# Kernel optimization log

Hardware: AMD Instinct MI355X
Metric: run time of the kernel (lower is better)

## Reference

```python
import jax, jax.numpy as jnp
import numpy as np

EMBED_DIM = 1024
NUM_HEADS = 16
HEAD_DIM = EMBED_DIM // NUM_HEADS


def setup_inputs() -> dict:
    key = jax.random.key(0)
    ks = jax.random.split(key, 9)
    B, N, D = 2, 2048, EMBED_DIM
    s = 1.0 / np.sqrt(D)
    return {
        "x": jax.random.normal(ks[0], (B, N, D), jnp.float32),
        "Wq": jax.random.normal(ks[1], (D, D), jnp.float32) * s,
        "bq": jax.random.normal(ks[2], (D,), jnp.float32) * 0.01,
        "Wk": jax.random.normal(ks[3], (D, D), jnp.float32) * s,
        "bk": jax.random.normal(ks[4], (D,), jnp.float32) * 0.01,
        "Wv": jax.random.normal(ks[5], (D, D), jnp.float32) * s,
        "bv": jax.random.normal(ks[6], (D,), jnp.float32) * 0.01,
        "Wo": jax.random.normal(ks[7], (D, D), jnp.float32) * s,
        "bo": jax.random.normal(ks[8], (D,), jnp.float32) * 0.01,
    }


def reference(x, Wq, bq, Wk, bk, Wv, bv, Wo, bo):
    B, N, D = x.shape
    H, Hd = NUM_HEADS, HEAD_DIM
    # QKV projections (Linear: x @ W^T + b), split heads -> [B, H, N, Hd]
    q = (x @ Wq.T + bq).reshape(B, N, H, Hd).transpose(0, 2, 1, 3)
    k = (x @ Wk.T + bk).reshape(B, N, H, Hd).transpose(0, 2, 1, 3)
    v = (x @ Wv.T + bv).reshape(B, N, H, Hd).transpose(0, 2, 1, 3)
    scale = 1.0 / np.sqrt(Hd)
    scores = jnp.einsum("bhqd,bhkd->bhqk", q, k) * scale  # [B,H,N,N]
    attn = jax.nn.softmax(scores.astype(jnp.float32), axis=-1).astype(scores.dtype)
    out = jnp.einsum("bhqk,bhkd->bhqd", attn, v)  # [B,H,N,Hd]
    out = out.transpose(0, 2, 1, 3).reshape(B, N, D)
    return out @ Wo.T + bo
```

## Files before the change

kernel.cpp:

```cpp
#include <hip/hip_runtime.h>
#include <hip/hip_bf16.h>

typedef __attribute__((ext_vector_type(8))) short short8;
typedef __attribute__((ext_vector_type(4))) float f32x4;
typedef __attribute__((ext_vector_type(4))) unsigned short us4;

static __device__ __forceinline__ unsigned short f2bf(float f) {
    union { float f; unsigned u; } v; v.f = f;
    unsigned r = (v.u + 0x7FFFu + ((v.u >> 16) & 1u)) >> 16;
    return (unsigned short)r;
}
static __device__ __forceinline__ unsigned pk2(float a, float b) {
    union { float f; unsigned u; } x, y; x.f = a; y.f = b;
    unsigned lo = (x.u + 0x7FFFu + ((x.u >> 16) & 1u)) >> 16;
    unsigned hi = (y.u + 0x7FFFu + ((y.u >> 16) & 1u)) >> 16;
    return lo | (hi << 16);
}
static __device__ __forceinline__ unsigned pk2f(float a, float b) {
    union { float f; unsigned u; } x, y; x.f = a; y.f = b;
    return ((x.u + 0x8000u) >> 16) | ((y.u + 0x8000u) & 0xFFFF0000u);
}

#if __has_builtin(__builtin_amdgcn_exp2f)
#define EXP2(x) __builtin_amdgcn_exp2f(x)
#else
#define EXP2(x) exp2f(x)
#endif

static __device__ __forceinline__ void gld16(const unsigned short* g, unsigned short* l) {
    __builtin_amdgcn_global_load_lds(
        (const __attribute__((address_space(1))) void*)g,
        (__attribute__((address_space(3))) void*)l, 16, 0, 0);
}

#define QSCALE (0.125f * 1.44269504f)

__global__ __launch_bounds__(256) void convert_all(
    const float* __restrict__ x,  const float* __restrict__ wq,
    const float* __restrict__ wk, const float* __restrict__ wv,
    const float* __restrict__ wo, const float* __restrict__ bq,
    const float* __restrict__ bk, const float* __restrict__ bv,
    unsigned short* __restrict__ xbf, unsigned short* __restrict__ wqkv,
    unsigned short* __restrict__ wobf, float* __restrict__ bqkv)
{
    const int NX4 = (4096 * 1024) / 4;
    const int NW4 = (1024 * 1024) / 4;
    int i = blockIdx.x * 256 + threadIdx.x;
    if (i < NX4) {
        float4 v = ((const float4*)x)[i];
        us4 o = { f2bf(v.x), f2bf(v.y), f2bf(v.z), f2bf(v.w) };
        ((us4*)xbf)[i] = o;
    } else if (i < NX4 + 3 * NW4) {
        int j = i - NX4;
        const float* src = (j < NW4) ? wq + 4 * j
                         : (j < 2 * NW4) ? wk + 4 * (j - NW4)
                         : wv + 4 * (j - 2 * NW4);
        float4 v = *(const float4*)src;
        us4 o = { f2bf(v.x), f2bf(v.y), f2bf(v.z), f2bf(v.w) };
        ((us4*)wqkv)[j] = o;
    } else if (i < NX4 + 4 * NW4) {
        int j = i - NX4 - 3 * NW4;
        float4 v = ((const float4*)wo)[j];
        us4 o = { f2bf(v.x), f2bf(v.y), f2bf(v.z), f2bf(v.w) };
        ((us4*)wobf)[j] = o;
    } else if (i < NX4 + 4 * NW4 + 768) {
        int j = i - NX4 - 4 * NW4;
        const float* src = (j < 256) ? bq + 4 * j
                         : (j < 512) ? bk + 4 * (j - 256)
                         : bv + 4 * (j - 512);
        ((float4*)bqkv)[j] = *(const float4*)src;
    }
}

template <int MODE>
__global__ __launch_bounds__(256) void gemm_bt(
    const unsigned short* __restrict__ A, const unsigned short* __restrict__ B,
    const float* __restrict__ bias,
    unsigned short* __restrict__ Qb, unsigned short* __restrict__ Kb,
    unsigned short* __restrict__ Vtb, float* __restrict__ Cout, int Mtiles)
{
    __shared__ __attribute__((aligned(16))) unsigned short As[8192];
    __shared__ __attribute__((aligned(16))) unsigned short Bs[8192];
    const int tid = threadIdx.x, lane = tid & 63, wave = tid >> 6;
    const int bm = blockIdx.x % Mtiles, bn = blockIdx.x / Mtiles;
    const int m0 = bm * 128, n0 = bn * 128;
    const int wr = wave >> 1, wc = wave & 1;
    const int lo = lane & 15, g = lane >> 4;

    f32x4 acc[4][4];
#pragma unroll
    for (int i = 0; i < 4; ++i)
#pragma unroll
        for (int j = 0; j < 4; ++j) acc[i][j] = (f32x4){0.f, 0.f, 0.f, 0.f};

    for (int kt = 0; kt < 16; ++kt) {
        const int k0 = kt * 64;
#pragma unroll
        for (int p = 0; p < 4; ++p) {
            int off = (p * 256 + tid) * 8;
            int k8l = off >> 10, m = (off >> 3) & 127;
            const unsigned short* srcA;
            if (MODE == 0) {
                srcA = A + (size_t)(m0 + m) * 1024 + k0 + k8l * 8;
            } else {
                int gr = m0 + m, b = gr >> 11, n = gr & 2047;
                srcA = A + ((size_t)((b << 4) + kt) * 2048 + n) * 64 + k8l * 8;
            }
            gld16(srcA, &As[off]);
            gld16(B + (size_t)(n0 + m) * 1024 + k0 + k8l * 8, &Bs[off]);
        }
        __syncthreads();
        short8 af[4][2], bf[4][2];
#pragma unroll
        for (int i = 0; i < 4; ++i)
#pragma unroll
            for (int kc = 0; kc < 2; ++kc) {
                af[i][kc] = *(const short8*)&As[((kc * 4 + g) * 128 + wr * 64 + i * 16 + lo) * 8];
                bf[i][kc] = *(const short8*)&Bs[((kc * 4 + g) * 128 + wc * 64 + i * 16 + lo) * 8];
            }
#pragma unroll
        for (int kc = 0; kc < 2; ++kc)
#pragma unroll
            for (int i = 0; i < 4; ++i)
#pragma unroll
                for (int j = 0; j < 4; ++j)
                    acc[i][j] = __builtin_amdgcn_mfma_f32_16x16x32_bf16(
                        af[i][kc], bf[j][kc], acc[i][j], 0, 0, 0);
        __syncthreads();
    }

    if (MODE == 0) {
        const int sect = n0 >> 10;
#pragma unroll
        for (int i = 0; i < 4; ++i)
#pragma unroll
            for (int j = 0; j < 4; ++j) {
                int gc = n0 + wc * 64 + j * 16 + lo;
                int d = gc & 1023, h = d >> 6, hd = d & 63;
                float bv = bias[gc];
                int nb = m0 + wr * 64 + i * 16 + g * 4;
                int b = nb >> 11, n = nb & 2047;
                size_t hb = (size_t)((b << 4) + h) * 131072;
                if (sect == 0) {
#pragma unroll
                    for (int r = 0; r < 4; ++r)
                        Qb[hb + (size_t)(n + r) * 64 + hd] =
                            f2bf((acc[i][j][r] + bv) * QSCALE);
                } else if (sect == 1) {
#pragma unroll
                    for (int r = 0; r < 4; ++r)
                        Kb[hb + (size_t)(hd >> 3) * 16384 + (size_t)(n + r) * 8 + (hd & 7)] =
                            f2bf(acc[i][j][r] + bv);
                } else {
                    uint2 w;
                    w.x = pk2(acc[i][j][0] + bv, acc[i][j][1] + bv);
                    w.y = pk2(acc[i][j][2] + bv, acc[i][j][3] + bv);
                    *(uint2*)&Vtb[hb + (size_t)(n >> 3) * 512 + (size_t)hd * 8 + (n & 7)] = w;
                }
            }
    } else {
#pragma unroll
        for (int i = 0; i < 4; ++i)
#pragma unroll
            for (int j = 0; j < 4; ++j)
#pragma unroll
                for (int r = 0; r < 4; ++r) {
                    int gr = m0 + wr * 64 + i * 16 + g * 4 + r;
                    int gc = n0 + wc * 64 + j * 16 + lo;
                    Cout[(size_t)gr * 1024 + gc] = acc[i][j][r] + bias[gc];
                }
    }
}

__global__ __launch_bounds__(256, 2) void attn_kernel(
    const unsigned short* __restrict__ Qb, const unsigned short* __restrict__ Kb,
    const unsigned short* __restrict__ Vtb, unsigned short* __restrict__ Ob)
{
    __shared__ __attribute__((aligned(16))) unsigned short Ks[8192];
    __shared__ __attribute__((aligned(16))) unsigned short Vs[8192];
    __shared__ __attribute__((aligned(16))) unsigned short PT[4 * 32 * 136];
    const int tid = threadIdx.x, lane = tid & 63, wave = tid >> 6;
    const int lo = lane & 15, g = lane >> 4;
    const int bh = blockIdx.x >> 4, qt = blockIdx.x & 15;
    const size_t base = (size_t)bh * 131072;
    const int q0w = qt * 128 + wave * 32;

    short8 aq[2][2];
#pragma unroll
    for (int rb = 0; rb < 2; ++rb) {
        const unsigned short* qp = Qb + base + (size_t)(q0w + rb * 16 + lo) * 64 + g * 8;
        aq[rb][0] = *(const short8*)qp;
        aq[rb][1] = *(const short8*)(qp + 32);
    }
    f32x4 o[2][4];
    float l[2] = {0.f, 0.f};
#pragma unroll
    for (int rb = 0; rb < 2; ++rb)
#pragma unroll
        for (int c = 0; c < 4; ++c) o[rb][c] = (f32x4){0.f, 0.f, 0.f, 0.f};
    unsigned short* myP = PT + wave * (32 * 136);
    const unsigned short* Kg = Kb + base;
    const unsigned short* Vg = Vtb + base;

    for (int kt = 0; kt < 16; ++kt) {
        const int k0 = kt * 128;
#pragma unroll
        for (int i = 0; i < 4; ++i) {
            int off = (wave * 4 + i) * 512 + lane * 8;
            gld16(Kg + (size_t)(off >> 10) * 16384 + k0 * 8 + (off & 1023), &Ks[off]);
            gld16(Vg + (size_t)k0 * 64 + off, &Vs[off]);
        }
        __syncthreads();

#pragma unroll
        for (int ct = 0; ct < 8; ++ct) {
            short8 kf0 = *(const short8*)&Ks[(size_t)g * 1024 + (ct * 16 + lo) * 8];
            short8 kf1 = *(const short8*)&Ks[(size_t)(4 + g) * 1024 + (ct * 16 + lo) * 8];
#pragma unroll
            for (int rb = 0; rb < 2; ++rb) {
                f32x4 z = (f32x4){0.f, 0.f, 0.f, 0.f};
                f32x4 s = __builtin_amdgcn_mfma_f32_16x16x32_bf16(kf0, aq[rb][0], z, 0, 0, 0);
                s = __builtin_amdgcn_mfma_f32_16x16x32_bf16(kf1, aq[rb][1], s, 0, 0, 0);
                float p0 = EXP2(s[0]), p1 = EXP2(s[1]);
                float p2 = EXP2(s[2]), p3 = EXP2(s[3]);
                l[rb] += (p0 + p1) + (p2 + p3);
                uint2 w; w.x = pk2f(p0, p1); w.y = pk2f(p2, p3);
                *(uint2*)&myP[(rb * 16 + lo) * 136 + ct * 16 + g * 4] = w;
            }
        }
#pragma unroll
        for (int kc = 0; kc < 4; ++kc) {
            short8 bp0 = *(const short8*)&myP[lo * 136 + kc * 32 + g * 8];
            short8 bp1 = *(const short8*)&myP[(16 + lo) * 136 + kc * 32 + g * 8];
#pragma unroll
            for (int c = 0; c < 4; ++c) {
                short8 vf = *(const short8*)&Vs[(kc * 4 + g) * 512 + (c * 16 + lo) * 8];
                o[0][c] = __builtin_amdgcn_mfma_f32_16x16x32_bf16(vf, bp0, o[0][c], 0, 0, 0);
                o[1][c] = __builtin_amdgcn_mfma_f32_16x16x32_bf16(vf, bp1, o[1][c], 0, 0, 0);
            }
        }
        __syncthreads();
    }

    float inv[2];
#pragma unroll
    for (int rb = 0; rb < 2; ++rb) {
        float v = l[rb];
        v += __shfl_xor(v, 16);
        v += __shfl_xor(v, 32);
        inv[rb] = 1.f / v;
    }
#pragma unroll
    for (int rb = 0; rb < 2; ++rb)
#pragma unroll
        for (int c = 0; c < 4; ++c) {
            uint2 w;
            w.x = pk2(o[rb][c][0] * inv[rb], o[rb][c][1] * inv[rb]);
            w.y = pk2(o[rb][c][2] * inv[rb], o[rb][c][3] * inv[rb]);
            *(uint2*)&Ob[base + (size_t)(q0w + rb * 16 + lo) * 64 + c * 16 + g * 4] = w;
        }
}

extern "C" void kernel_launch(void* const* d_in, const int* in_sizes, int n_in,
                              void* d_out, int out_size, void* d_ws, size_t ws_size,
                              hipStream_t stream) {
    const float* x  = (const float*)d_in[0];
    const float* Wq = (const float*)d_in[1];
    const float* bq = (const float*)d_in[2];
    const float* Wk = (const float*)d_in[3];
    const float* bk = (const float*)d_in[4];
    const float* Wv = (const float*)d_in[5];
    const float* bv = (const float*)d_in[6];
    const float* Wo = (const float*)d_in[7];
    const float* bo = (const float*)d_in[8];
    float* out = (float*)d_out;

    char* ws = (char*)d_ws;
    unsigned short* xbf  = (unsigned short*)ws;
    unsigned short* wqkv = (unsigned short*)(ws + 8388608);
    unsigned short* wobf = (unsigned short*)(ws + 14680064);
    float*          bqkv = (float*)(ws + 16777216);
    unsigned short* Qb   = (unsigned short*)(ws + 16789504);
    unsigned short* Kb   = (unsigned short*)(ws + 16789504 + 8388608);
    unsigned short* Vtb  = (unsigned short*)(ws + 16789504 + 2 * 8388608);
    unsigned short* Ob   = (unsigned short*)(ws + 16789504 + 3 * 8388608);

    convert_all<<<8195, 256, 0, stream>>>(x, Wq, Wk, Wv, Wo, bq, bk, bv,
                                          xbf, wqkv, wobf, bqkv);
    gemm_bt<0><<<32 * 24, 256, 0, stream>>>(xbf, wqkv, bqkv, Qb, Kb, Vtb, nullptr, 32);
    attn_kernel<<<512, 256, 0, stream>>>(Qb, Kb, Vtb, Ob);
    gemm_bt<1><<<32 * 8, 256, 0, stream>>>(Ob, wobf, bo, nullptr, nullptr, nullptr, out, 32);
}
```

Before: 248.5 us.

## Double-buffer GEMM tiles, retile output GEMM, read K/V directly in attention

The GEMM kernel is templated on tile shape and now double-buffers its LDS tiles, prefetching the next K-slice while computing the current one. The output projection switches to 64x128 tiles so the grid doubles to 512 blocks and fills more CUs. The attention kernel drops its shared-memory K/V staging and both barriers, loading K and V fragments straight from global memory (relying on L1/L2), and reorders block indexing so neighbouring blocks share a head. These changes trade LDS traffic and synchronisation for more global loads and larger LDS footprint in the GEMM, and remove the 2-block occupancy hint on attention.

```diff
diff --git a/kernel.cpp b/kernel.cpp
--- a/kernel.cpp
+++ b/kernel.cpp
@@ -72,33 +72,36 @@
     }
 }
 
-template <int MODE>
+template <int MODE, int BM, int BN, int WR, int WC>
 __global__ __launch_bounds__(256) void gemm_bt(
     const unsigned short* __restrict__ A, const unsigned short* __restrict__ B,
     const float* __restrict__ bias,
     unsigned short* __restrict__ Qb, unsigned short* __restrict__ Kb,
     unsigned short* __restrict__ Vtb, float* __restrict__ Cout, int Mtiles)
 {
-    __shared__ __attribute__((aligned(16))) unsigned short As[8192];
-    __shared__ __attribute__((aligned(16))) unsigned short Bs[8192];
+    constexpr int WM = BM / WR, WN = BN / WC;
+    constexpr int IT = WM / 16, JT = WN / 16;
+    constexpr int ASZ = BM * 64, BSZ = BN * 64;
+    __shared__ __attribute__((aligned(16))) unsigned short As[2 * ASZ];
+    __shared__ __attribute__((aligned(16))) unsigned short Bs[2 * BSZ];
     const int tid = threadIdx.x, lane = tid & 63, wave = tid >> 6;
     const int bm = blockIdx.x % Mtiles, bn = blockIdx.x / Mtiles;
-    const int m0 = bm * 128, n0 = bn * 128;
-    const int wr = wave >> 1, wc = wave & 1;
+    const int m0 = bm * BM, n0 = bn * BN;
+    const int wr = wave / WC, wc = wave % WC;
     const int lo = lane & 15, g = lane >> 4;
 
-    f32x4 acc[4][4];
-#pragma unroll
-    for (int i = 0; i < 4; ++i)
-#pragma unroll
-        for (int j = 0; j < 4; ++j) acc[i][j] = (f32x4){0.f, 0.f, 0.f, 0.f};
-
-    for (int kt = 0; kt < 16; ++kt) {
+    f32x4 acc[IT][JT];
+#pragma unroll
+    for (int i = 0; i < IT; ++i)
+#pragma unroll
+        for (int j = 0; j < JT; ++j) acc[i][j] = (f32x4){0.f, 0.f, 0.f, 0.f};
+
+    auto stage = [&](int kt, int buf) {
         const int k0 = kt * 64;
 #pragma unroll
-        for (int p = 0; p < 4; ++p) {
-            int off = (p * 256 + tid) * 8;
-            int k8l = off >> 10, m = (off >> 3) & 127;
+        for (int p = 0; p < BM / 32; ++p) {
+            int off = p * 2048 + tid * 8;
+            int k8l = off / (BM * 8), m = (off >> 3) & (BM - 1);
             const unsigned short* srcA;
             if (MODE == 0) {
                 srcA = A + (size_t)(m0 + m) * 1024 + k0 + k8l * 8;
@@ -106,24 +109,39 @@
                 int gr = m0 + m, b = gr >> 11, n = gr & 2047;
                 srcA = A + ((size_t)((b << 4) + kt) * 2048 + n) * 64 + k8l * 8;
             }
-            gld16(srcA, &As[off]);
-            gld16(B + (size_t)(n0 + m) * 1024 + k0 + k8l * 8, &Bs[off]);
-        }
-        __syncthreads();
-        short8 af[4][2], bf[4][2];
-#pragma unroll
-        for (int i = 0; i < 4; ++i)
-#pragma unroll
-            for (int kc = 0; kc < 2; ++kc) {
-                af[i][kc] = *(const short8*)&As[((kc * 4 + g) * 128 + wr * 64 + i * 16 + lo) * 8];
-                bf[i][kc] = *(const short8*)&Bs[((kc * 4 + g) * 128 + wc * 64 + i * 16 + lo) * 8];
-            }
+            gld16(srcA, &As[buf * ASZ + off]);
+        }
+#pragma unroll
+        for (int p = 0; p < BN / 32; ++p) {
+            int off = p * 2048 + tid * 8;
+            int k8l = off / (BN * 8), m = (off >> 3) & (BN - 1);
+            gld16(B + (size_t)(n0 + m) * 1024 + k0 + k8l * 8, &Bs[buf * BSZ + off]);
+        }
+    };
+
+    stage(0, 0);
+    __syncthreads();
+    for (int kt = 0; kt < 16; ++kt) {
+        const int cur = kt & 1;
+        if (kt < 15) stage(kt + 1, cur ^ 1);
+        short8 af[IT][2], bf[JT][2];
+#pragma unroll
+        for (int kc = 0; kc < 2; ++kc) {
+#pragma unroll
+            for (int i = 0; i < IT; ++i)
+                af[i][kc] = *(const short8*)&As[cur * ASZ +
+                    ((kc * 4 + g) * BM + wr * WM + i * 16 + lo) * 8];
+#pragma unroll
+            for (int j = 0; j < JT; ++j)
+                bf[j][kc] = *(const short8*)&Bs[cur * BSZ +
+                    ((kc * 4 + g) * BN + wc * WN + j * 16 + lo) * 8];
+        }
 #pragma unroll
         for (int kc = 0; kc < 2; ++kc)
 #pragma unroll
-            for (int i = 0; i < 4; ++i)
-#pragma unroll
-                for (int j = 0; j < 4; ++j)
+            for (int i = 0; i < IT; ++i)
+#pragma unroll
+                for (int j = 0; j < JT; ++j)
                     acc[i][j] = __builtin_amdgcn_mfma_f32_16x16x32_bf16(
                         af[i][kc], bf[j][kc], acc[i][j], 0, 0, 0);
         __syncthreads();
@@ -132,13 +150,13 @@
     if (MODE == 0) {
         const int sect = n0 >> 10;
 #pragma unroll
-        for (int i = 0; i < 4; ++i)
-#pragma unroll
-            for (int j = 0; j < 4; ++j) {
-                int gc = n0 + wc * 64 + j * 16 + lo;
+        for (int i = 0; i < IT; ++i)
+#pragma unroll
+            for (int j = 0; j < JT; ++j) {
+                int gc = n0 + wc * WN + j * 16 + lo;
                 int d = gc & 1023, h = d >> 6, hd = d & 63;
                 float bv = bias[gc];
-                int nb = m0 + wr * 64 + i * 16 + g * 4;
+                int nb = m0 + wr * WM + i * 16 + g * 4;
                 int b = nb >> 11, n = nb & 2047;
                 size_t hb = (size_t)((b << 4) + h) * 131072;
                 if (sect == 0) {
@@ -160,28 +178,26 @@
             }
     } else {
 #pragma unroll
-        for (int i = 0; i < 4; ++i)
-#pragma unroll
-            for (int j = 0; j < 4; ++j)
+        for (int i = 0; i < IT; ++i)
+#pragma unroll
+            for (int j = 0; j < JT; ++j)
 #pragma unroll
                 for (int r = 0; r < 4; ++r) {
-                    int gr = m0 + wr * 64 + i * 16 + g * 4 + r;
-                    int gc = n0 + wc * 64 + j * 16 + lo;
+                    int gr = m0 + wr * WM + i * 16 + g * 4 + r;
+                    int gc = n0 + wc * WN + j * 16 + lo;
                     Cout[(size_t)gr * 1024 + gc] = acc[i][j][r] + bias[gc];
                 }
     }
 }
 
-__global__ __launch_bounds__(256, 2) void attn_kernel(
+__global__ __launch_bounds__(256) void attn_kernel(
     const unsigned short* __restrict__ Qb, const unsigned short* __restrict__ Kb,
     const unsigned short* __restrict__ Vtb, unsigned short* __restrict__ Ob)
 {
-    __shared__ __attribute__((aligned(16))) unsigned short Ks[8192];
-    __shared__ __attribute__((aligned(16))) unsigned short Vs[8192];
     __shared__ __attribute__((aligned(16))) unsigned short PT[4 * 32 * 136];
     const int tid = threadIdx.x, lane = tid & 63, wave = tid >> 6;
     const int lo = lane & 15, g = lane >> 4;
-    const int bh = blockIdx.x >> 4, qt = blockIdx.x & 15;
+    const int bh = blockIdx.x & 31, qt = blockIdx.x >> 5;
     const size_t base = (size_t)bh * 131072;
     const int q0w = qt * 128 + wave * 32;
 
@@ -205,17 +221,10 @@
     for (int kt = 0; kt < 16; ++kt) {
         const int k0 = kt * 128;
 #pragma unroll
-        for (int i = 0; i < 4; ++i) {
-            int off = (wave * 4 + i) * 512 + lane * 8;
-            gld16(Kg + (size_t)(off >> 10) * 16384 + k0 * 8 + (off & 1023), &Ks[off]);
-            gld16(Vg + (size_t)k0 * 64 + off, &Vs[off]);
-        }
-        __syncthreads();
-
-#pragma unroll
         for (int ct = 0; ct < 8; ++ct) {
-            short8 kf0 = *(const short8*)&Ks[(size_t)g * 1024 + (ct * 16 + lo) * 8];
-            short8 kf1 = *(const short8*)&Ks[(size_t)(4 + g) * 1024 + (ct * 16 + lo) * 8];
+            const unsigned short* kp = Kg + (size_t)(k0 + ct * 16 + lo) * 8;
+            short8 kf0 = *(const short8*)(kp + (size_t)g * 16384);
+            short8 kf1 = *(const short8*)(kp + (size_t)(4 + g) * 16384);
 #pragma unroll
             for (int rb = 0; rb < 2; ++rb) {
                 f32x4 z = (f32x4){0.f, 0.f, 0.f, 0.f};
@@ -234,12 +243,12 @@
             short8 bp1 = *(const short8*)&myP[(16 + lo) * 136 + kc * 32 + g * 8];
 #pragma unroll
             for (int c = 0; c < 4; ++c) {
-                short8 vf = *(const short8*)&Vs[(kc * 4 + g) * 512 + (c * 16 + lo) * 8];
+                short8 vf = *(const short8*)(Vg +
+                    (size_t)((k0 >> 3) + kc * 4 + g) * 512 + (size_t)(c * 16 + lo) * 8);
                 o[0][c] = __builtin_amdgcn_mfma_f32_16x16x32_bf16(vf, bp0, o[0][c], 0, 0, 0);
                 o[1][c] = __builtin_amdgcn_mfma_f32_16x16x32_bf16(vf, bp1, o[1][c], 0, 0, 0);
             }
         }
-        __syncthreads();
     }
 
     float inv[2];
@@ -287,7 +296,9 @@
 
     convert_all<<<8195, 256, 0, stream>>>(x, Wq, Wk, Wv, Wo, bq, bk, bv,
                                           xbf, wqkv, wobf, bqkv);
-    gemm_bt<0><<<32 * 24, 256, 0, stream>>>(xbf, wqkv, bqkv, Qb, Kb, Vtb, nullptr, 32);
+    gemm_bt<0, 128, 128, 2, 2><<<32 * 24, 256, 0, stream>>>(
+        xbf, wqkv, bqkv, Qb, Kb, Vtb, nullptr, 32);
     attn_kernel<<<512, 256, 0, stream>>>(Qb, Kb, Vtb, Ob);
-    gemm_bt<1><<<32 * 8, 256, 0, stream>>>(Ob, wobf, bo, nullptr, nullptr, nullptr, out, 32);
-}
+    gemm_bt<1, 64, 128, 1, 4><<<64 * 8, 256, 0, stream>>>(
+        Ob, wobf, bo, nullptr, nullptr, nullptr, out, 64);
+}
```

After: 308.5 us. +24.1%, slower.
